# Optimization experiments

Measured on AMD Instinct MI355X. Metric: run time of the kernel, lower is better.

The kernel has to match this reference:

```python
import jax, jax.numpy as jnp
import numpy as np

B, H, S, D = 2, 16, 2048, 128
TEMPERATURE = 11.313708498984761  # sqrt(128)


def setup_inputs() -> dict:
    key = jax.random.key(0)
    kq, kk, kv = jax.random.split(key, 3)
    q = jax.random.normal(kq, (B, H, S, D), dtype=jnp.float32)
    k = jax.random.normal(kk, (B, H, S, D), dtype=jnp.float32)
    v = jax.random.normal(kv, (B, H, S, D), dtype=jnp.float32)
    # causal (lower-triangular) mask; 0 == masked, matching mask.eq(0) semantics
    mask = jnp.broadcast_to(
        jnp.tril(jnp.ones((S, S), dtype=jnp.int32))[None, None], (B, 1, S, S)
    )
    return {"q": q, "k": k, "v": v, "mask": mask}


def reference(q, k, v, mask):
    # attn = q @ k^T / temperature   -> [B,H,S,S]
    attn = jnp.einsum("bhqd,bhkd->bhqk", q, k) / TEMPERATURE
    masked = mask == 0  # True where masked out
    attn = jnp.where(masked, -jnp.inf, attn)
    attn = jax.nn.softmax(attn, axis=-1)
    attn = jnp.where(masked, 0.0, attn)
    # output = attn @ v -> [B,H,S,D]
    return jnp.einsum("bhqk,bhkd->bhqd", attn, v)
```

## Files before the change

kernel.cpp:

```cpp
#include <hip/hip_runtime.h>
#include <hip/hip_bf16.h>

#define NB   2
#define NH   16
#define NBH  (NB*NH)
#define SEQ  2048
#define DH   128

#define KBLK 64
#define QB   64
#define QW   16
#define KS   136
#define VS   72
#define PS   72

typedef short  short8    __attribute__((ext_vector_type(8)));
typedef short  short4v   __attribute__((ext_vector_type(4)));
typedef unsigned short ushort8_t __attribute__((ext_vector_type(8)));
typedef float  f32x4     __attribute__((ext_vector_type(4)));

constexpr float INV_T = 0.08838834764831845f;
constexpr float LOG2E = 1.4426950408889634f;
constexpr float QSCL  = INV_T * LOG2E;
constexpr float NEG   = -1e30f;
constexpr float DEFER = 8.0f;

__device__ __forceinline__ unsigned short f2b(float x) {
    union { float f; unsigned u; } c; c.f = x;
    unsigned r = c.u + 0x7FFFu + ((c.u >> 16) & 1u);
    return (unsigned short)(r >> 16);
}

__device__ __forceinline__ unsigned pack2(float lo, float hi) {
    return (unsigned)f2b(lo) | ((unsigned)f2b(hi) << 16);
}

__device__ __forceinline__ short4v mk4(unsigned lo, unsigned hi) {
    union { unsigned u[2]; short4v s; } x; x.u[0] = lo; x.u[1] = hi; return x.s;
}

__device__ __forceinline__ f32x4 mfma16(short4v a, short4v b, f32x4 c) {
#if __has_builtin(__builtin_amdgcn_mfma_f32_16x16x16bf16_1k)
    return __builtin_amdgcn_mfma_f32_16x16x16bf16_1k(a, b, c, 0, 0, 0);
#else
    f32x4 d;
    asm("v_mfma_f32_16x16x16_bf16 %0, %1, %2, %3"
        : "=v"(d) : "v"(a), "v"(b), "0"(c));
    return d;
#endif
}

__device__ __forceinline__ void gload_lds16(const void* g, void* l) {
    __builtin_amdgcn_global_load_lds(
        (const __attribute__((address_space(1))) unsigned int*)g,
        (__attribute__((address_space(3))) unsigned int*)l, 16, 0, 0);
}

__global__ __launch_bounds__(256)
void prep_k(const float* __restrict__ K, unsigned short* __restrict__ Kb) {
    size_t i = ((size_t)blockIdx.x * 256 + threadIdx.x) * 8;
    float4 a = *(const float4*)(K + i);
    float4 b = *(const float4*)(K + i + 4);
    ushort8_t o;
    o[0]=f2b(a.x); o[1]=f2b(a.y); o[2]=f2b(a.z); o[3]=f2b(a.w);
    o[4]=f2b(b.x); o[5]=f2b(b.y); o[6]=f2b(b.z); o[7]=f2b(b.w);
    *(ushort8_t*)(Kb + i) = o;
}

__global__ __launch_bounds__(256)
void prep_v(const float* __restrict__ V, unsigned short* __restrict__ Vt) {
    __shared__ unsigned short T[64][72];
    const int bid = blockIdx.x;
    const int dt = bid & 1, st = (bid >> 1) & 31, bh = bid >> 6;
    const int s0 = st * 64, d0 = dt * 64;
    const float* vb = V + (size_t)bh * SEQ * DH;
    const int tid = threadIdx.x;
    #pragma unroll
    for (int u = 0; u < 4; ++u) {
        int f = tid + 256 * u;
        int sl = f >> 4, c4 = f & 15;
        float4 x = *(const float4*)(vb + (size_t)(s0 + sl) * DH + d0 + c4 * 4);
        T[c4*4+0][sl] = f2b(x.x); T[c4*4+1][sl] = f2b(x.y);
        T[c4*4+2][sl] = f2b(x.z); T[c4*4+3][sl] = f2b(x.w);
    }
    __syncthreads();
    unsigned short* vo = Vt + (size_t)bh * DH * SEQ;
    const int dr = tid >> 2, ch = tid & 3;
    ushort8_t w0 = *(const ushort8_t*)&T[dr][ch*16];
    ushort8_t w1 = *(const ushort8_t*)&T[dr][ch*16 + 8];
    *(ushort8_t*)(vo + (size_t)(d0+dr)*SEQ + s0 + ch*16)     = w0;
    *(ushort8_t*)(vo + (size_t)(d0+dr)*SEQ + s0 + ch*16 + 8) = w1;
}

__global__ __launch_bounds__(256, 2)
void attn_fwd3(const float* __restrict__ Q,
               const unsigned short* __restrict__ Kb,
               const unsigned short* __restrict__ Vt,
               float* __restrict__ O)
{
    __shared__ __align__(16) unsigned short Ksh[2][64 * 128];
    __shared__ __align__(16) unsigned short Vsh[2][128 * 64];

    const int bid  = blockIdx.x;
    const int qblk = 15 - (bid >> 5);
    const int bh   = bid & 31;
    const int tid  = threadIdx.x;
    const int wid  = tid >> 6;
    const int lane = tid & 63;
    const int l15  = lane & 15;
    const int l4   = lane >> 4;
    const int rx   = l15 & 7;

    const size_t base = (size_t)bh * SEQ * DH;
    const unsigned short* Kbh = Kb + base;
    const unsigned short* Vth = Vt + base;

    const int qbase = qblk * 128 + wid * 32;
    const int nt    = 2 * qblk + 2;
    const int qr0   = qbase + l15;
    const int qr1   = qbase + 16 + l15;

    auto stage = [&](int bufi, int tt) {
        const int kv0 = tt * KBLK;
        {
            const int sl = lane & 15, rr = lane >> 4;
            #pragma unroll
            for (int i = 0; i < 4; ++i) {
                int row = wid * 16 + i * 4 + rr;
                int ss  = sl ^ (row & 7);
                gload_lds16(Kbh + (size_t)(kv0 + row) * DH + ss * 8,
                            &Ksh[bufi][(wid * 16 + i * 4) * 128]);
            }
        }
        {
            const int sl = lane & 7, rr = lane >> 3;
            #pragma unroll
            for (int i = 0; i < 4; ++i) {
                int row = wid * 32 + i * 8 + rr;
                int ss  = sl ^ (row & 7);
                gload_lds16(Vth + (size_t)row * SEQ + kv0 + ss * 8,
                            &Vsh[bufi][(wid * 32 + i * 8) * 64]);
            }
        }
    };

    short8 aq0[4], aq1[4];
    {
        const float* qp0 = Q + base + (size_t)qr0 * DH + 8 * l4;
        const float* qp1 = Q + base + (size_t)qr1 * DH + 8 * l4;
        #pragma unroll
        for (int kb = 0; kb < 4; ++kb) {
            float4 x0 = *(const float4*)(qp0 + 32 * kb);
            float4 x1 = *(const float4*)(qp0 + 32 * kb + 4);
            float4 y0 = *(const float4*)(qp1 + 32 * kb);
            float4 y1 = *(const float4*)(qp1 + 32 * kb + 4);
            short8 a, b;
            a[0] = (short)f2b(x0.x * QSCL); a[1] = (short)f2b(x0.y * QSCL);
            a[2] = (short)f2b(x0.z * QSCL); a[3] = (short)f2b(x0.w * QSCL);
            a[4] = (short)f2b(x1.x * QSCL); a[5] = (short)f2b(x1.y * QSCL);
            a[6] = (short)f2b(x1.z * QSCL); a[7] = (short)f2b(x1.w * QSCL);
            b[0] = (short)f2b(y0.x * QSCL); b[1] = (short)f2b(y0.y * QSCL);
            b[2] = (short)f2b(y0.z * QSCL); b[3] = (short)f2b(y0.w * QSCL);
            b[4] = (short)f2b(y1.x * QSCL); b[5] = (short)f2b(y1.y * QSCL);
            b[6] = (short)f2b(y1.z * QSCL); b[7] = (short)f2b(y1.w * QSCL);
            aq0[kb] = a; aq1[kb] = b;
        }
    }

    f32x4 acc0[8], acc1[8];
    #pragma unroll
    for (int i = 0; i < 8; ++i) {
        acc0[i] = (f32x4){0.f, 0.f, 0.f, 0.f};
        acc1[i] = (f32x4){0.f, 0.f, 0.f, 0.f};
    }
    float mrun0 = NEG, lrun0 = 0.f;
    float mrun1 = NEG, lrun1 = 0.f;

    stage(0, 0);

    for (int t = 0; t < nt; ++t) {
        const int cur = t & 1;
        const int kvb = t * KBLK;
        asm volatile("s_waitcnt vmcnt(0)" ::: "memory");
        __syncthreads();
        if (t + 1 < nt) stage(cur ^ 1, t + 1);

        if (kvb <= qbase + 31) {
            const unsigned short* Kc = Ksh[cur];
            const unsigned short* Vc = Vsh[cur];

            f32x4 sf0[4], sf1[4];
            __builtin_amdgcn_s_setprio(1);
            #pragma unroll
            for (int f = 0; f < 4; ++f) {
                f32x4 c0 = (f32x4){0.f, 0.f, 0.f, 0.f};
                f32x4 c1 = (f32x4){0.f, 0.f, 0.f, 0.f};
                const int row = 16 * f + l15;
                #pragma unroll
                for (int kb = 0; kb < 4; ++kb) {
                    short8 bk = *(const short8*)&Kc[row * 128 + ((4 * kb + l4) ^ rx) * 8];
                    c0 = __builtin_amdgcn_mfma_f32_16x16x32_bf16(bk, aq0[kb], c0, 0, 0, 0);
                    c1 = __builtin_amdgcn_mfma_f32_16x16x32_bf16(bk, aq1[kb], c1, 0, 0, 0);
                }
                sf0[f] = c0; sf1[f] = c1;
            }
            __builtin_amdgcn_s_setprio(0);

            if (kvb + KBLK - 1 > qbase) {
                #pragma unroll
                for (int f = 0; f < 4; ++f) {
                    #pragma unroll
                    for (int j = 0; j < 4; ++j) {
                        const int kv = kvb + 16 * f + 4 * l4 + j;
                        if (kv > qr0) sf0[f][j] = NEG;
                        if (kv > qr1) sf1[f][j] = NEG;
                    }
                }
            }

            float pmax0, pmax1;
            {
                float a0 = fmaxf(fmaxf(sf0[0][0], sf0[0][1]), fmaxf(sf0[0][2], sf0[0][3]));
                float a1 = fmaxf(fmaxf(sf0[1][0], sf0[1][1]), fmaxf(sf0[1][2], sf0[1][3]));
                float a2 = fmaxf(fmaxf(sf0[2][0], sf0[2][1]), fmaxf(sf0[2][2], sf0[2][3]));
                float a3 = fmaxf(fmaxf(sf0[3][0], sf0[3][1]), fmaxf(sf0[3][2], sf0[3][3]));
                pmax0 = fmaxf(fmaxf(a0, a1), fmaxf(a2, a3));
                float b0 = fmaxf(fmaxf(sf1[0][0], sf1[0][1]), fmaxf(sf1[0][2], sf1[0][3]));
                float b1 = fmaxf(fmaxf(sf1[1][0], sf1[1][1]), fmaxf(sf1[1][2], sf1[1][3]));
                float b2 = fmaxf(fmaxf(sf1[2][0], sf1[2][1]), fmaxf(sf1[2][2], sf1[2][3]));
                float b3 = fmaxf(fmaxf(sf1[3][0], sf1[3][1]), fmaxf(sf1[3][2], sf1[3][3]));
                pmax1 = fmaxf(fmaxf(b0, b1), fmaxf(b2, b3));
            }
            pmax0 = fmaxf(pmax0, __shfl_xor(pmax0, 16));
            pmax0 = fmaxf(pmax0, __shfl_xor(pmax0, 32));
            pmax1 = fmaxf(pmax1, __shfl_xor(pmax1, 16));
            pmax1 = fmaxf(pmax1, __shfl_xor(pmax1, 32));

            if (__any((pmax0 > mrun0 + DEFER) || (pmax1 > mrun1 + DEFER))) {
                float mn0 = fmaxf(mrun0, pmax0), mn1 = fmaxf(mrun1, pmax1);
                float s0 = exp2f(mrun0 - mn0),   s1 = exp2f(mrun1 - mn1);
                mrun0 = mn0; mrun1 = mn1;
                lrun0 *= s0; lrun1 *= s1;
                #pragma unroll
                for (int i = 0; i < 8; ++i)
                    #pragma unroll
                    for (int j = 0; j < 4; ++j) {
                        acc0[i][j] *= s0;
                        acc1[i][j] *= s1;
                    }
            }

            unsigned pa0[4], pb0_[4], pa1[4], pb1_[4];
            float rs0 = 0.f, rs1 = 0.f;
            #pragma unroll
            for (int f = 0; f < 4; ++f) {
                float p00 = exp2f(sf0[f][0] - mrun0), p01 = exp2f(sf0[f][1] - mrun0);
                float p02 = exp2f(sf0[f][2] - mrun0), p03 = exp2f(sf0[f][3] - mrun0);
                float p10 = exp2f(sf1[f][0] - mrun1), p11 = exp2f(sf1[f][1] - mrun1);
                float p12 = exp2f(sf1[f][2] - mrun1), p13 = exp2f(sf1[f][3] - mrun1);
                rs0 += (p00 + p01) + (p02 + p03);
                rs1 += (p10 + p11) + (p12 + p13);
                pa0[f]  = pack2(p00, p01); pb0_[f] = pack2(p02, p03);
                pa1[f]  = pack2(p10, p11); pb1_[f] = pack2(p12, p13);
            }
            rs0 += __shfl_xor(rs0, 16); rs0 += __shfl_xor(rs0, 32);
            rs1 += __shfl_xor(rs1, 16); rs1 += __shfl_xor(rs1, 32);
            lrun0 += rs0; lrun1 += rs1;

            #pragma unroll
            for (int f = 0; f < 4; ++f) {
                short4v pf0 = mk4(pa0[f], pb0_[f]);
                short4v pf1 = mk4(pa1[f], pb1_[f]);
                __builtin_amdgcn_s_setprio(1);
                #pragma unroll
                for (int db = 0; db < 8; ++db) {
                    const int row = 16 * db + l15;
                    short4v va = *(const short4v*)
                        &Vc[row * 64 + ((2 * f + (l4 >> 1)) ^ rx) * 8 + (l4 & 1) * 4];
                    acc0[db] = mfma16(va, pf0, acc0[db]);
                    acc1[db] = mfma16(va, pf1, acc1[db]);
                }
                __builtin_amdgcn_s_setprio(0);
            }
        }
    }

    const float inv0 = 1.f / lrun0;
    const float inv1 = 1.f / lrun1;
    float* op0 = O + base + (size_t)qr0 * DH + 4 * l4;
    float* op1 = O + base + (size_t)qr1 * DH + 4 * l4;
    #pragma unroll
    for (int db = 0; db < 8; ++db) {
        float4 v0, v1;
        v0.x = acc0[db][0] * inv0; v0.y = acc0[db][1] * inv0;
        v0.z = acc0[db][2] * inv0; v0.w = acc0[db][3] * inv0;
        v1.x = acc1[db][0] * inv1; v1.y = acc1[db][1] * inv1;
        v1.z = acc1[db][2] * inv1; v1.w = acc1[db][3] * inv1;
        *(float4*)(op0 + 16 * db) = v0;
        *(float4*)(op1 + 16 * db) = v1;
    }
}

__global__ __launch_bounds__(256)
void attn_fwd(const float* __restrict__ Q, const float* __restrict__ K,
              const float* __restrict__ V, float* __restrict__ O)
{
    __shared__ __align__(16) unsigned short KshL[KBLK * KS];
    __shared__ __align__(16) unsigned short VshL[DH * VS];
    __shared__ __align__(16) unsigned short PshL[4][QW * PS];

    const int bid  = blockIdx.x;
    const int qblk = bid & 31;
    const int bh   = bid >> 5;
    const int tid  = threadIdx.x;
    const int wid  = tid >> 6;
    const int lane = tid & 63;
    const int l15  = lane & 15;
    const int l4   = lane >> 4;

    const size_t base  = (size_t)bh * SEQ * DH;
    const int    qbase = qblk * QB + wid * QW;

    short8 aq[4];
    {
        const float* qp = Q + base + (size_t)(qbase + l15) * DH + 8 * l4;
        #pragma unroll
        for (int kb = 0; kb < 4; ++kb) {
            float4 x0 = *(const float4*)(qp + 32 * kb);
            float4 x1 = *(const float4*)(qp + 32 * kb + 4);
            short8 a;
            a[0] = (short)f2b(x0.x * INV_T); a[1] = (short)f2b(x0.y * INV_T);
            a[2] = (short)f2b(x0.z * INV_T); a[3] = (short)f2b(x0.w * INV_T);
            a[4] = (short)f2b(x1.x * INV_T); a[5] = (short)f2b(x1.y * INV_T);
            a[6] = (short)f2b(x1.z * INV_T); a[7] = (short)f2b(x1.w * INV_T);
            aq[kb] = a;
        }
    }
    f32x4 acc[8];
    #pragma unroll
    for (int i = 0; i < 8; ++i) acc[i] = (f32x4){0.f, 0.f, 0.f, 0.f};
    float mrun[4], lrun[4];
    #pragma unroll
    for (int j = 0; j < 4; ++j) { mrun[j] = NEG; lrun[j] = 0.f; }

    const int ntiles = qblk + 1;
    for (int t = 0; t < ntiles; ++t) {
        const int kvb = t * KBLK;
        #pragma unroll
        for (int i = 0; i < 8; ++i) {
            int f  = tid + 256 * i;
            int kv = f >> 5, c4 = f & 31;
            float4 x = *(const float4*)(K + base + (size_t)(kvb + kv) * DH + 4 * c4);
            ushort4 b4;
            b4.x = f2b(x.x); b4.y = f2b(x.y); b4.z = f2b(x.z); b4.w = f2b(x.w);
            *(ushort4*)&KshL[kv * KS + 4 * c4] = b4;
        }
        {
            const int dd  = tid & 127;
            const int kvg = (tid >> 7) * 8;
            #pragma unroll
            for (int p = 0; p < 4; ++p) {
                const int kvL = p * 16 + kvg;
                const float* vp = V + base + (size_t)(kvb + kvL) * DH + dd;
                float x[8];
                #pragma unroll
                for (int j = 0; j < 8; ++j) x[j] = vp[(size_t)j * DH];
                ushort4 lo, hi;
                lo.x = f2b(x[0]); lo.y = f2b(x[1]); lo.z = f2b(x[2]); lo.w = f2b(x[3]);
                hi.x = f2b(x[4]); hi.y = f2b(x[5]); hi.z = f2b(x[6]); hi.w = f2b(x[7]);
                *(ushort4*)&VshL[dd * VS + kvL]     = lo;
                *(ushort4*)&VshL[dd * VS + kvL + 4] = hi;
            }
        }
        __syncthreads();
        if (kvb <= qbase + QW - 1) {
            f32x4 sf[4];
            #pragma unroll
            for (int f = 0; f < 4; ++f) {
                f32x4 c = (f32x4){0.f, 0.f, 0.f, 0.f};
                #pragma unroll
                for (int kb = 0; kb < 4; ++kb) {
                    short8 bk = *(const short8*)&KshL[(16 * f + l15) * KS + 32 * kb + 8 * l4];
                    c = __builtin_amdgcn_mfma_f32_16x16x32_bf16(aq[kb], bk, c, 0, 0, 0);
                }
                sf[f] = c;
            }
            float pmax[4] = {NEG, NEG, NEG, NEG};
            #pragma unroll
            for (int f = 0; f < 4; ++f) {
                const int col = kvb + 16 * f + l15;
                #pragma unroll
                for (int j = 0; j < 4; ++j) {
                    const int row = qbase + 4 * l4 + j;
                    float val = (col <= row) ? sf[f][j] : NEG;
                    sf[f][j] = val;
                    pmax[j] = fmaxf(pmax[j], val);
                }
            }
            #pragma unroll
            for (int j = 0; j < 4; ++j) {
                #pragma unroll
                for (int off = 8; off > 0; off >>= 1)
                    pmax[j] = fmaxf(pmax[j], __shfl_xor(pmax[j], off));
            }
            float scl[4], rsum[4];
            #pragma unroll
            for (int j = 0; j < 4; ++j) {
                float mn = fmaxf(mrun[j], pmax[j]);
                scl[j]  = exp2f((mrun[j] - mn) * LOG2E);
                mrun[j] = mn;
                rsum[j] = 0.f;
            }
            #pragma unroll
            for (int f = 0; f < 4; ++f) {
                #pragma unroll
                for (int j = 0; j < 4; ++j) {
                    float pv = exp2f((sf[f][j] - mrun[j]) * LOG2E);
                    sf[f][j] = pv;
                    rsum[j] += pv;
                }
            }
            #pragma unroll
            for (int j = 0; j < 4; ++j) {
                #pragma unroll
                for (int off = 8; off > 0; off >>= 1)
                    rsum[j] += __shfl_xor(rsum[j], off);
                lrun[j] = lrun[j] * scl[j] + rsum[j];
            }
            #pragma unroll
            for (int i = 0; i < 8; ++i)
                #pragma unroll
                for (int j = 0; j < 4; ++j)
                    acc[i][j] *= scl[j];
            #pragma unroll
            for (int f = 0; f < 4; ++f)
                #pragma unroll
                for (int j = 0; j < 4; ++j)
                    PshL[wid][(4 * l4 + j) * PS + 16 * f + l15] = f2b(sf[f][j]);
            #pragma unroll
            for (int kb = 0; kb < 2; ++kb) {
                short8 pa = *(const short8*)&PshL[wid][l15 * PS + 32 * kb + 8 * l4];
                #pragma unroll
                for (int db = 0; db < 8; ++db) {
                    short8 bv = *(const short8*)&VshL[(16 * db + l15) * VS + 32 * kb + 8 * l4];
                    acc[db] = __builtin_amdgcn_mfma_f32_16x16x32_bf16(pa, bv, acc[db], 0, 0, 0);
                }
            }
        }
        __syncthreads();
    }
    float inv[4];
    #pragma unroll
    for (int j = 0; j < 4; ++j) inv[j] = 1.f / lrun[j];
    float* op = O + base + (size_t)qbase * DH;
    #pragma unroll
    for (int db = 0; db < 8; ++db)
        #pragma unroll
        for (int j = 0; j < 4; ++j)
            op[(size_t)(4 * l4 + j) * DH + 16 * db + l15] = acc[db][j] * inv[j];
}

extern "C" void kernel_launch(void* const* d_in, const int* in_sizes, int n_in,
                              void* d_out, int out_size, void* d_ws, size_t ws_size,
                              hipStream_t stream) {
    const float* q = (const float*)d_in[0];
    const float* k = (const float*)d_in[1];
    const float* v = (const float*)d_in[2];
    float* o = (float*)d_out;

    const size_t elems = (size_t)NBH * SEQ * DH;
    const size_t need  = elems * 2 * sizeof(unsigned short);
    if (ws_size >= need) {
        unsigned short* Kb = (unsigned short*)d_ws;
        unsigned short* Vt = Kb + elems;
        prep_k<<<dim3((unsigned)(elems / (256 * 8))), dim3(256), 0, stream>>>(k, Kb);
        prep_v<<<dim3(NBH * (SEQ / 64) * (DH / 64)), dim3(256), 0, stream>>>(v, Vt);
        attn_fwd3<<<dim3(NBH * 16), dim3(256), 0, stream>>>(q, Kb, Vt, o);
    } else {
        attn_fwd<<<dim3(NBH * 32), dim3(256), 0, stream>>>(q, k, v, o);
    }
}
```

Before: 245.7 us.

## Skip fully masked key subtiles, use hardware bf16 pack, defer max shuffles

On diagonal tiles, the QK, softmax and PV loops now stop at the last 16-key fragment that any row in the warp can see, so fully masked fragments are never computed. The software bf16 rounding is replaced by the v_cvt_pk_bf16_f32 instruction. The cross-lane shuffles for the row max now run only when the rescale branch is taken, using per-lane maxima for the vote. The early-break loops add divergence-free but data-dependent control flow that may hurt register allocation or unrolling, and the per-lane vote changes when the rescale triggers.

```diff
diff --git a/kernel.cpp b/kernel.cpp
--- a/kernel.cpp
+++ b/kernel.cpp
@@ -31,8 +31,10 @@
     return (unsigned short)(r >> 16);
 }
 
-__device__ __forceinline__ unsigned pack2(float lo, float hi) {
-    return (unsigned)f2b(lo) | ((unsigned)f2b(hi) << 16);
+__device__ __forceinline__ unsigned cvtpk(float lo, float hi) {
+    unsigned r;
+    asm("v_cvt_pk_bf16_f32 %0, %1, %2" : "=v"(r) : "v"(lo), "v"(hi));
+    return r;
 }
 
 __device__ __forceinline__ short4v mk4(unsigned lo, unsigned hi) {
@@ -119,6 +121,7 @@
     const int nt    = 2 * qblk + 2;
     const int qr0   = qbase + l15;
     const int qr1   = qbase + 16 + l15;
+    const int qtop  = qbase + 31;
 
     auto stage = [&](int bufi, int tt) {
         const int kv0 = tt * KBLK;
@@ -185,14 +188,20 @@
         __syncthreads();
         if (t + 1 < nt) stage(cur ^ 1, t + 1);
 
-        if (kvb <= qbase + 31) {
+        if (kvb <= qtop) {
             const unsigned short* Kc = Ksh[cur];
             const unsigned short* Vc = Vsh[cur];
+            const bool fok1 = (kvb + 16 <= qtop);
+            const bool fok2 = (kvb + 32 <= qtop);
+            const bool fok3 = (kvb + 48 <= qtop);
 
             f32x4 sf0[4], sf1[4];
             __builtin_amdgcn_s_setprio(1);
             #pragma unroll
             for (int f = 0; f < 4; ++f) {
+                if (f == 1 && !fok1) break;
+                if (f == 2 && !fok2) break;
+                if (f == 3 && !fok3) break;
                 f32x4 c0 = (f32x4){0.f, 0.f, 0.f, 0.f};
                 f32x4 c1 = (f32x4){0.f, 0.f, 0.f, 0.f};
                 const int row = 16 * f + l15;
@@ -205,10 +214,12 @@
                 sf0[f] = c0; sf1[f] = c1;
             }
             __builtin_amdgcn_s_setprio(0);
+            const int nf = fok3 ? 4 : (fok2 ? 3 : (fok1 ? 2 : 1));
 
             if (kvb + KBLK - 1 > qbase) {
                 #pragma unroll
                 for (int f = 0; f < 4; ++f) {
+                    if (f >= nf) break;
                     #pragma unroll
                     for (int j = 0; j < 4; ++j) {
                         const int kv = kvb + 16 * f + 4 * l4 + j;
@@ -218,27 +229,23 @@
                 }
             }
 
-            float pmax0, pmax1;
-            {
-                float a0 = fmaxf(fmaxf(sf0[0][0], sf0[0][1]), fmaxf(sf0[0][2], sf0[0][3]));
-                float a1 = fmaxf(fmaxf(sf0[1][0], sf0[1][1]), fmaxf(sf0[1][2], sf0[1][3]));
-                float a2 = fmaxf(fmaxf(sf0[2][0], sf0[2][1]), fmaxf(sf0[2][2], sf0[2][3]));
-                float a3 = fmaxf(fmaxf(sf0[3][0], sf0[3][1]), fmaxf(sf0[3][2], sf0[3][3]));
-                pmax0 = fmaxf(fmaxf(a0, a1), fmaxf(a2, a3));
-                float b0 = fmaxf(fmaxf(sf1[0][0], sf1[0][1]), fmaxf(sf1[0][2], sf1[0][3]));
-                float b1 = fmaxf(fmaxf(sf1[1][0], sf1[1][1]), fmaxf(sf1[1][2], sf1[1][3]));
-                float b2 = fmaxf(fmaxf(sf1[2][0], sf1[2][1]), fmaxf(sf1[2][2], sf1[2][3]));
-                float b3 = fmaxf(fmaxf(sf1[3][0], sf1[3][1]), fmaxf(sf1[3][2], sf1[3][3]));
-                pmax1 = fmaxf(fmaxf(b0, b1), fmaxf(b2, b3));
-            }
-            pmax0 = fmaxf(pmax0, __shfl_xor(pmax0, 16));
-            pmax0 = fmaxf(pmax0, __shfl_xor(pmax0, 32));
-            pmax1 = fmaxf(pmax1, __shfl_xor(pmax1, 16));
-            pmax1 = fmaxf(pmax1, __shfl_xor(pmax1, 32));
-
-            if (__any((pmax0 > mrun0 + DEFER) || (pmax1 > mrun1 + DEFER))) {
-                float mn0 = fmaxf(mrun0, pmax0), mn1 = fmaxf(mrun1, pmax1);
-                float s0 = exp2f(mrun0 - mn0),   s1 = exp2f(mrun1 - mn1);
+            float lm0 = NEG, lm1 = NEG;
+            #pragma unroll
+            for (int f = 0; f < 4; ++f) {
+                if (f >= nf) break;
+                lm0 = fmaxf(lm0, fmaxf(fmaxf(sf0[f][0], sf0[f][1]),
+                                       fmaxf(sf0[f][2], sf0[f][3])));
+                lm1 = fmaxf(lm1, fmaxf(fmaxf(sf1[f][0], sf1[f][1]),
+                                       fmaxf(sf1[f][2], sf1[f][3])));
+            }
+
+            if (__any((lm0 > mrun0 + DEFER) || (lm1 > mrun1 + DEFER))) {
+                float pm0 = fmaxf(lm0, __shfl_xor(lm0, 16));
+                pm0 = fmaxf(pm0, __shfl_xor(pm0, 32));
+                float pm1 = fmaxf(lm1, __shfl_xor(lm1, 16));
+                pm1 = fmaxf(pm1, __shfl_xor(pm1, 32));
+                float mn0 = fmaxf(mrun0, pm0), mn1 = fmaxf(mrun1, pm1);
+                float s0 = exp2f(mrun0 - mn0), s1 = exp2f(mrun1 - mn1);
                 mrun0 = mn0; mrun1 = mn1;
                 lrun0 *= s0; lrun1 *= s1;
                 #pragma unroll
@@ -254,14 +261,15 @@
             float rs0 = 0.f, rs1 = 0.f;
             #pragma unroll
             for (int f = 0; f < 4; ++f) {
+                if (f >= nf) break;
                 float p00 = exp2f(sf0[f][0] - mrun0), p01 = exp2f(sf0[f][1] - mrun0);
                 float p02 = exp2f(sf0[f][2] - mrun0), p03 = exp2f(sf0[f][3] - mrun0);
                 float p10 = exp2f(sf1[f][0] - mrun1), p11 = exp2f(sf1[f][1] - mrun1);
                 float p12 = exp2f(sf1[f][2] - mrun1), p13 = exp2f(sf1[f][3] - mrun1);
                 rs0 += (p00 + p01) + (p02 + p03);
                 rs1 += (p10 + p11) + (p12 + p13);
-                pa0[f]  = pack2(p00, p01); pb0_[f] = pack2(p02, p03);
-                pa1[f]  = pack2(p10, p11); pb1_[f] = pack2(p12, p13);
+                pa0[f]  = cvtpk(p00, p01); pb0_[f] = cvtpk(p02, p03);
+                pa1[f]  = cvtpk(p10, p11); pb1_[f] = cvtpk(p12, p13);
             }
             rs0 += __shfl_xor(rs0, 16); rs0 += __shfl_xor(rs0, 32);
             rs1 += __shfl_xor(rs1, 16); rs1 += __shfl_xor(rs1, 32);
@@ -269,6 +277,7 @@
 
             #pragma unroll
             for (int f = 0; f < 4; ++f) {
+                if (f >= nf) break;
                 short4v pf0 = mk4(pa0[f], pb0_[f]);
                 short4v pf1 = mk4(pa1[f], pb1_[f]);
                 __builtin_amdgcn_s_setprio(1);
```

After: 245.5 us. No clear change (-0.1%).
